# Kernel tuning notes

Hardware: AMD Instinct MI355X
Metric: run time of the kernel (lower is better)

The kernel has to match this reference:

```python
import jax, jax.numpy as jnp
import numpy as np

B, P, COV, H, S = 1024, 96, 31, 1024, 100  # batch, pred_len, cov_dim, hidden, num_samples
IN = COV + 1


def setup_inputs() -> dict:
    key = jax.random.key(0)
    ks = jax.random.split(key, 16)
    sc = 1.0 / np.sqrt(H)
    return {
        "covariates": jax.random.normal(ks[0], (B, P, COV), jnp.float32),
        "initial_value": jax.random.normal(ks[1], (B, 1), jnp.float32),
        "noise": jax.random.normal(ks[2], (P, S, B), jnp.float32),
        "h_init": jax.random.normal(ks[3], (2, B, H), jnp.float32) * 0.1,
        "c_init": jax.random.normal(ks[4], (2, B, H), jnp.float32) * 0.1,
        "W_ih0": jax.random.normal(ks[5], (4 * H, IN), jnp.float32) * sc,
        "W_hh0": jax.random.normal(ks[6], (4 * H, H), jnp.float32) * sc,
        "b_ih0": jax.random.normal(ks[7], (4 * H,), jnp.float32) * sc,
        "b_hh0": jax.random.normal(ks[8], (4 * H,), jnp.float32) * sc,
        "W_ih1": jax.random.normal(ks[9], (4 * H, H), jnp.float32) * sc,
        "W_hh1": jax.random.normal(ks[10], (4 * H, H), jnp.float32) * sc,
        "b_ih1": jax.random.normal(ks[11], (4 * H,), jnp.float32) * sc,
        "b_hh1": jax.random.normal(ks[12], (4 * H,), jnp.float32) * sc,
        "W_proj": jax.random.normal(ks[13], (2, H), jnp.float32) * sc,
        "b_proj": jax.random.normal(ks[14], (2,), jnp.float32) * sc,
    }


def _lstm_cell(x, h, c, W_ih, W_hh, b_ih, b_hh):
    # PyTorch gate order: i, f, g, o
    gates = x @ W_ih.T + h @ W_hh.T + b_ih + b_hh  # [B, 4H]
    i, f, g, o = jnp.split(gates, 4, axis=-1)
    i, f, o = jax.nn.sigmoid(i), jax.nn.sigmoid(f), jax.nn.sigmoid(o)
    g = jnp.tanh(g)
    c_new = f * c + i * g
    h_new = o * jnp.tanh(c_new)
    return h_new, c_new


def reference(covariates, initial_value, noise, h_init, c_init,
              W_ih0, W_hh0, b_ih0, b_hh0, W_ih1, W_hh1, b_ih1, b_hh1,
              W_proj, b_proj):
    def step(carry, inp):
        h0, c0, h1, c1, cur = carry
        cov_t, noise_t = inp  # [B, COV], [S, B]
        x = jnp.concatenate([cur[:, None], cov_t], axis=-1)  # [B, IN]
        h0, c0 = _lstm_cell(x, h0, c0, W_ih0, W_hh0, b_ih0, b_hh0)
        h1, c1 = _lstm_cell(h0, h1, c1, W_ih1, W_hh1, b_ih1, b_hh1)
        params = h1 @ W_proj.T + b_proj  # [B, 2]
        mu = params[:, 0]
        sigma = jax.nn.softplus(params[:, 1]) + 1e-6
        samples = mu[None, :] + sigma[None, :] * noise_t  # [S, B]
        cur = samples[0]
        return (h0, c0, h1, c1, cur), (params, samples)

    carry0 = (h_init[0], c_init[0], h_init[1], c_init[1], initial_value[:, 0])
    xs = (jnp.swapaxes(covariates, 0, 1), noise)  # time-major
    _, (all_params, all_samples) = jax.lax.scan(step, carry0, xs)
    all_params = jnp.swapaxes(all_params, 0, 1)       # [B, P, 2]
    all_samples = jnp.transpose(all_samples, (1, 2, 0))  # [S, B, P]
    return all_params, all_samples
```

## Files before the change

kernel.cpp:

```cpp
#include <hip/hip_runtime.h>
#include <stdint.h>

#define Bsz 1024
#define Hsz 1024
#define Psteps 96
#define Ssamp 100
#define COVn 31

typedef __attribute__((ext_vector_type(8))) short short8;
typedef __attribute__((ext_vector_type(4))) float f32x4;

__device__ inline unsigned short f2bf(float f) {
    union { float f; unsigned u; } v; v.f = f;
    unsigned r = v.u + 0x7FFFu + ((v.u >> 16) & 1u);
    return (unsigned short)(r >> 16);
}

__device__ inline float sigm(float x) { return 1.f / (1.f + __expf(-x)); }
__device__ inline float tanh_f(float x) { return 2.f / (1.f + __expf(-2.f * x)) - 1.f; }
__device__ inline float softplusf(float x) {
    return fmaxf(x, 0.f) + log1pf(__expf(-fabsf(x)));
}

__device__ inline void gld16(const unsigned short* g, unsigned short* l) {
    auto gp = (const __attribute__((address_space(1))) unsigned int*)(const unsigned int*)g;
    auto lp = (__attribute__((address_space(3))) unsigned int*)(unsigned int*)l;
    __builtin_amdgcn_global_load_lds(gp, lp, 16, 0, 0);
}

__device__ inline void stage_tile(const unsigned short* __restrict__ src, int rowStride,
                                  int row0, int k0, unsigned short* ldsBase, int tid) {
    #pragma unroll
    for (int i = 0; i < 4; ++i) {
        int c = i * 256 + tid;
        int row = c >> 3, s = c & 7;
        int col = ((s ^ (row & 7)) << 3) + k0;
        gld16(src + (size_t)(row0 + row) * rowStride + col, ldsBase + c * 8);
    }
}

__global__ void prep_weights(const float* __restrict__ Wih0, const float* __restrict__ Whh0,
                             const float* __restrict__ Wih1, const float* __restrict__ Whh1,
                             const float* __restrict__ bih0, const float* __restrict__ bhh0,
                             const float* __restrict__ bih1, const float* __restrict__ bhh1,
                             unsigned short* __restrict__ W0cat, unsigned short* __restrict__ W1cat,
                             float* __restrict__ bias0, float* __restrict__ bias1) {
    const size_t N0 = (size_t)4096 * 1088;
    const size_t N1 = (size_t)4096 * 2048;
    const size_t total = N0 + N1 + 8192;
    for (size_t e = (size_t)blockIdx.x * 256 + threadIdx.x; e < total; e += (size_t)gridDim.x * 256) {
        if (e < N0) {
            int gh = (int)(e / 1088), col = (int)(e % 1088);
            int src = ((gh & 3) << 10) + (gh >> 2);
            float v;
            if (col < 32) v = Wih0[(size_t)src * 32 + col];
            else if (col < 64) v = 0.f;
            else v = Whh0[(size_t)src * 1024 + (col - 64)];
            W0cat[e] = f2bf(v);
        } else if (e < N0 + N1) {
            size_t m = e - N0;
            int gh = (int)(m >> 11), col = (int)(m & 2047);
            int src = ((gh & 3) << 10) + (gh >> 2);
            float v = (col < 1024) ? Wih1[(size_t)src * 1024 + col]
                                   : Whh1[(size_t)src * 1024 + (col - 1024)];
            W1cat[m] = f2bf(v);
        } else {
            size_t m = e - N0 - N1;
            int which = (int)(m >> 12);
            int gh = (int)(m & 4095);
            int src = ((gh & 3) << 10) + (gh >> 2);
            if (which == 0) bias0[gh] = bih0[src] + bhh0[src];
            else            bias1[gh] = bih1[src] + bhh1[src];
        }
    }
}

__global__ void prep_state(const float* __restrict__ hinit, const float* __restrict__ cinit,
                           unsigned short* __restrict__ hb0, unsigned short* __restrict__ hb1,
                           float* __restrict__ c0, float* __restrict__ c1) {
    const size_t NM = (size_t)1024 * 1024;
    for (size_t e = (size_t)blockIdx.x * 256 + threadIdx.x; e < 4 * NM; e += (size_t)gridDim.x * 256) {
        if (e < NM) {
            hb0[e] = f2bf(hinit[e]);
        } else if (e < 2 * NM) {
            hb1[e - NM] = f2bf(hinit[e]);
        } else if (e < 3 * NM) {
            size_t j = e - 2 * NM; int h = (int)(j >> 10), b = (int)(j & 1023);
            c0[j] = cinit[(size_t)b * 1024 + h];
        } else {
            size_t j = e - 3 * NM; int h = (int)(j >> 10), b = (int)(j & 1023);
            c1[j] = cinit[NM + (size_t)b * 1024 + h];
        }
    }
}

template<int CELL>
__global__ __launch_bounds__(256) void lstm_step(
        int t,
        const float* __restrict__ cov, const float* __restrict__ initv,
        const float* __restrict__ noise, const float* __restrict__ bproj,
        const float* __restrict__ wproj,
        const unsigned short* __restrict__ WA,
        const float* __restrict__ biasH,
        const unsigned short* __restrict__ hA,
        const unsigned short* __restrict__ hB,
        unsigned short* __restrict__ hOut,
        float* __restrict__ cws,
        float* __restrict__ pbufPartial,
        float* __restrict__ outParams) {
    __shared__ __align__(16) char smem[131072];

    const int tid = threadIdx.x;
    const int m_tile = blockIdx.x & 31;
    const int n_tile = blockIdx.x >> 5;
    const int m0 = m_tile * 128;
    const int hc0 = m_tile * 32;
    const int b0 = n_tile * 128;
    const int lane = tid & 63;
    const int wid = tid >> 6;
    const int wm = wid >> 1, wn = wid & 1;
    const int NIT = (CELL == 0) ? 17 : 32;

    auto stageIt = [&](int j) {
        unsigned short* Ab = (unsigned short*)(smem + (j & 3) * 16384);
        unsigned short* Bb = (unsigned short*)(smem + 65536 + (j & 3) * 16384);
        if (CELL == 0) {
            stage_tile(WA, 1088, m0, j * 64, Ab, tid);
            if (j > 0) stage_tile(hB, 1024, b0, (j - 1) * 64, Bb, tid);
        } else {
            stage_tile(WA, 2048, m0, j * 64, Ab, tid);
            if (j < 16) stage_tile(hA, 1024, b0, j * 64, Bb, tid);
            else        stage_tile(hB, 1024, b0, (j - 16) * 64, Bb, tid);
        }
    };

    stageIt(0);
    stageIt(1);
    if (CELL == 0) {
        float* pj = (float*)(smem + 114688);
        float* curF = (float*)(smem + 114688 + 2048);
        if (t > 0) {
            int bl = tid >> 1, j = tid & 1;
            float s = bproj[j];
            #pragma unroll 8
            for (int m = 0; m < 32; ++m)
                s += pbufPartial[(size_t)((m << 10) + b0 + bl) * 2 + j];
            pj[tid] = s;
            if (m_tile == 0)
                outParams[((size_t)(b0 + bl) * Psteps + (t - 1)) * 2 + j] = s;
        }
        __syncthreads();
        if (tid < 128) {
            float cu;
            if (t == 0) {
                cu = initv[b0 + tid];
            } else {
                float p0 = pj[tid * 2 + 0], p1 = pj[tid * 2 + 1];
                cu = p0 + (softplusf(p1) + 1e-6f) * noise[(size_t)(t - 1) * (Ssamp * Bsz) + b0 + tid];
            }
            curF[tid] = cu;
        }
        __syncthreads();
        #pragma unroll
        for (int i = 0; i < 4; ++i) {
            int c = i * 256 + tid;
            int row = c >> 3, s = c & 7;
            int ts = s ^ (row & 7);
            short8 v;
            if (ts < 4) {
                const float* cr = cov + ((size_t)(b0 + row) * Psteps + t) * COVn;
                #pragma unroll
                for (int e = 0; e < 8; ++e) {
                    int col = ts * 8 + e;
                    float x = (col == 0) ? curF[row] : cr[col - 1];
                    v[e] = (short)f2bf(x);
                }
            } else {
                v = (short8){0, 0, 0, 0, 0, 0, 0, 0};
            }
            *(short8*)(smem + 65536 + c * 16) = v;
        }
    }
    __syncthreads();

    f32x4 acc[4][4];
    #pragma unroll
    for (int i = 0; i < 4; ++i)
        #pragma unroll
        for (int j = 0; j < 4; ++j) acc[i][j] = (f32x4){0.f, 0.f, 0.f, 0.f};

    for (int it = 0; it < NIT; ++it) {
        if (it + 2 < NIT) stageIt(it + 2);
        int rem = NIT - 1 - it;
        if (rem >= 2)      asm volatile("s_waitcnt vmcnt(16)" ::: "memory");
        else if (rem == 1) asm volatile("s_waitcnt vmcnt(8)" ::: "memory");
        else               asm volatile("s_waitcnt vmcnt(0)" ::: "memory");
        __builtin_amdgcn_s_barrier();
        asm volatile("" ::: "memory");
        const char* Abuf = smem + (it & 3) * 16384;
        const char* Bbuf = smem + 65536 + (it & 3) * 16384;
        __builtin_amdgcn_s_setprio(1);
        #pragma unroll
        for (int kh = 0; kh < 2; ++kh) {
            short8 af[4], bq[4];
            #pragma unroll
            for (int mf = 0; mf < 4; ++mf) {
                int row = wm * 64 + mf * 16 + (lane & 15);
                int slot = (kh * 4 + (lane >> 4)) ^ (row & 7);
                af[mf] = *(const short8*)(Abuf + row * 128 + slot * 16);
            }
            #pragma unroll
            for (int nf = 0; nf < 4; ++nf) {
                int row = wn * 64 + nf * 16 + (lane & 15);
                int slot = (kh * 4 + (lane >> 4)) ^ (row & 7);
                bq[nf] = *(const short8*)(Bbuf + row * 128 + slot * 16);
            }
            #pragma unroll
            for (int mf = 0; mf < 4; ++mf)
                #pragma unroll
                for (int nf = 0; nf < 4; ++nf)
                    acc[mf][nf] = __builtin_amdgcn_mfma_f32_16x16x32_bf16(af[mf], bq[nf], acc[mf][nf], 0, 0, 0);
        }
        __builtin_amdgcn_s_setprio(0);
    }
    __syncthreads();

    unsigned short* Ht = (unsigned short*)smem;
    float* part = (float*)(smem + 16384);
    float pp[4][2];
    if (CELL == 1) {
        #pragma unroll
        for (int nf = 0; nf < 4; ++nf) { pp[nf][0] = 0.f; pp[nf][1] = 0.f; }
    }
    #pragma unroll
    for (int mf = 0; mf < 4; ++mf) {
        int hl = wm * 16 + mf * 4 + (lane >> 4);
        int h = hc0 + hl;
        f32x4 bs = *(const f32x4*)&biasH[h * 4];
        #pragma unroll
        for (int nf = 0; nf < 4; ++nf) {
            int bl = wn * 64 + nf * 16 + (lane & 15);
            int b = b0 + bl;
            f32x4 v = acc[mf][nf];
            float gi = sigm(v.x + bs.x);
            float gf = sigm(v.y + bs.y);
            float gg = tanh_f(v.z + bs.z);
            float go = sigm(v.w + bs.w);
            size_t ci = (size_t)h * Bsz + b;
            float cn = gf * cws[ci] + gi * gg;
            cws[ci] = cn;
            float hn = go * tanh_f(cn);
            Ht[bl * 40 + hl] = f2bf(hn);
            if (CELL == 1) {
                pp[nf][0] += hn * wproj[h];
                pp[nf][1] += hn * wproj[Hsz + h];
            }
        }
    }
    if (CELL == 1) {
        #pragma unroll
        for (int nf = 0; nf < 4; ++nf)
            #pragma unroll
            for (int j = 0; j < 2; ++j) {
                float v = pp[nf][j];
                v += __shfl_xor(v, 16, 64);
                v += __shfl_xor(v, 32, 64);
                if (lane < 16)
                    part[((wm * 128) + wn * 64 + nf * 16 + lane) * 2 + j] = v;
            }
    }
    __syncthreads();
    {
        int row = tid >> 1, hf = tid & 1;
        short8 v0 = *(const short8*)&Ht[row * 40 + hf * 16];
        short8 v1 = *(const short8*)&Ht[row * 40 + hf * 16 + 8];
        *(short8*)&hOut[(size_t)(b0 + row) * Hsz + hc0 + hf * 16] = v0;
        *(short8*)&hOut[(size_t)(b0 + row) * Hsz + hc0 + hf * 16 + 8] = v1;
    }
    if (CELL == 1) {
        int bl = tid >> 1, j = tid & 1;
        pbufPartial[((size_t)m_tile * 1024 + b0 + bl) * 2 + j] =
            part[bl * 2 + j] + part[(128 + bl) * 2 + j];
    }
}

__global__ void tail_params(const float* __restrict__ pPart, const float* __restrict__ bproj,
                            float* __restrict__ dout, float* __restrict__ musig) {
    int idx = blockIdx.x * 256 + threadIdx.x;
    if (idx >= Bsz * Psteps) return;
    int b = idx / Psteps, t = idx % Psteps;
    float p0, p1;
    if (t == Psteps - 1) {
        p0 = bproj[0]; p1 = bproj[1];
        #pragma unroll 8
        for (int m = 0; m < 32; ++m) {
            p0 += pPart[(size_t)((m << 10) + b) * 2 + 0];
            p1 += pPart[(size_t)((m << 10) + b) * 2 + 1];
        }
        dout[(size_t)idx * 2 + 0] = p0;
        dout[(size_t)idx * 2 + 1] = p1;
    } else {
        p0 = dout[(size_t)idx * 2 + 0];
        p1 = dout[(size_t)idx * 2 + 1];
    }
    musig[(size_t)idx * 2 + 0] = p0;
    musig[(size_t)idx * 2 + 1] = softplusf(p1) + 1e-6f;
}

__global__ __launch_bounds__(256) void gen_samples(const float* __restrict__ noise,
                                                   const float* __restrict__ musig,
                                                   float* __restrict__ outS) {
    __shared__ float tile[16][97];
    int s = blockIdx.x >> 6;
    int b0 = (blockIdx.x & 63) << 4;
    int tid = threadIdx.x;
    for (int e = tid; e < Psteps * 16; e += 256) {
        int tt = e >> 4, b = e & 15;
        tile[b][tt] = noise[((size_t)tt * Ssamp + s) * Bsz + b0 + b];
    }
    __syncthreads();
    int b = tid >> 4, t0 = (tid & 15) * 6;
    const float* ms = musig + ((size_t)(b0 + b) * Psteps + t0) * 2;
    float* op = outS + ((size_t)s * Bsz + b0 + b) * Psteps + t0;
    #pragma unroll
    for (int k = 0; k < 6; ++k) {
        op[k] = ms[k * 2] + ms[k * 2 + 1] * tile[b][t0 + k];
    }
}

extern "C" void kernel_launch(void* const* d_in, const int* in_sizes, int n_in,
                              void* d_out, int out_size, void* d_ws, size_t ws_size,
                              hipStream_t stream) {
    const float* cov   = (const float*)d_in[0];
    const float* initv = (const float*)d_in[1];
    const float* noise = (const float*)d_in[2];
    const float* hinit = (const float*)d_in[3];
    const float* cinit = (const float*)d_in[4];
    const float* Wih0  = (const float*)d_in[5];
    const float* Whh0  = (const float*)d_in[6];
    const float* bih0  = (const float*)d_in[7];
    const float* bhh0  = (const float*)d_in[8];
    const float* Wih1  = (const float*)d_in[9];
    const float* Whh1  = (const float*)d_in[10];
    const float* bih1  = (const float*)d_in[11];
    const float* bhh1  = (const float*)d_in[12];
    const float* wproj = (const float*)d_in[13];
    const float* bproj = (const float*)d_in[14];
    float* dout = (float*)d_out;

    uint8_t* p = (uint8_t*)d_ws;
    auto alloc = [&](size_t bytes) { void* r = (void*)p; p += (bytes + 255) & ~(size_t)255; return r; };
    unsigned short* W0cat = (unsigned short*)alloc((size_t)4096 * 1088 * 2);
    unsigned short* W1cat = (unsigned short*)alloc((size_t)4096 * 2048 * 2);
    float* bias0 = (float*)alloc(4096 * 4);
    float* bias1 = (float*)alloc(4096 * 4);
    unsigned short* hb0 = (unsigned short*)alloc((size_t)2 * 1024 * 1024 * 2 + 256);
    unsigned short* hb1 = (unsigned short*)alloc((size_t)2 * 1024 * 1024 * 2 + 256);
    float* c0 = (float*)alloc((size_t)1024 * 1024 * 4);
    float* c1 = (float*)alloc((size_t)1024 * 1024 * 4);
    float* pbufPartial = (float*)alloc((size_t)32 * 1024 * 2 * 4);
    float* musig = (float*)alloc((size_t)1024 * 96 * 2 * 4);

    prep_weights<<<2048, 256, 0, stream>>>(Wih0, Whh0, Wih1, Whh1, bih0, bhh0, bih1, bhh1,
                                           W0cat, W1cat, bias0, bias1);
    prep_state<<<2048, 256, 0, stream>>>(hinit, cinit, hb0, hb1, c0, c1);

    const size_t HB = (size_t)1024 * 1024;
    for (int t = 0; t < Psteps; ++t) {
        const unsigned short* h0p = hb0 + (size_t)(t & 1) * HB;
        unsigned short* h0n = hb0 + (size_t)((t + 1) & 1) * HB;
        const unsigned short* h1p = hb1 + (size_t)(t & 1) * HB;
        unsigned short* h1n = hb1 + (size_t)((t + 1) & 1) * HB;
        lstm_step<0><<<256, 256, 0, stream>>>(t, cov, initv, noise, bproj, wproj,
                                              W0cat, bias0, nullptr, h0p, h0n, c0,
                                              pbufPartial, dout);
        lstm_step<1><<<256, 256, 0, stream>>>(t, cov, initv, noise, bproj, wproj,
                                              W1cat, bias1, h0n, h1p, h1n, c1,
                                              pbufPartial, dout);
    }
    tail_params<<<384, 256, 0, stream>>>(pbufPartial, bproj, dout, musig);
    gen_samples<<<6400, 256, 0, stream>>>(noise, musig, dout + (size_t)Bsz * Psteps * 2);
}
```

Measured before the change: 4.682 ms.

## Halve batch tile to 64, double-buffer LDS, launch 512 blocks per step

Each LSTM step block now covers 128 gate rows by 64 batch columns instead of 128, so the grid doubles to 512 blocks and more CUs are busy on a 256-CU part. LDS shrinks from 128KB to 48KB and the four-stage global_load_lds pipeline becomes a two-buffer scheme with a full __syncthreads per iteration, allowing two blocks per CU. The intent is better machine fill and occupancy. In exchange, the weight tile is re-read by twice as many blocks, and the shallower prefetch depth with an extra barrier per K step exposes more load latency.

```diff
diff --git a/kernel.cpp b/kernel.cpp
--- a/kernel.cpp
+++ b/kernel.cpp
@@ -28,10 +28,11 @@
     __builtin_amdgcn_global_load_lds(gp, lp, 16, 0, 0);
 }
 
+template<int CH>
 __device__ inline void stage_tile(const unsigned short* __restrict__ src, int rowStride,
                                   int row0, int k0, unsigned short* ldsBase, int tid) {
     #pragma unroll
-    for (int i = 0; i < 4; ++i) {
+    for (int i = 0; i < CH; ++i) {
         int c = i * 256 + tid;
         int row = c >> 3, s = c & 7;
         int col = ((s ^ (row & 7)) << 3) + k0;
@@ -95,7 +96,7 @@
 }
 
 template<int CELL>
-__global__ __launch_bounds__(256) void lstm_step(
+__global__ __launch_bounds__(256, 2) void lstm_step(
         int t,
         const float* __restrict__ cov, const float* __restrict__ initv,
         const float* __restrict__ noise, const float* __restrict__ bproj,
@@ -108,49 +109,50 @@
         float* __restrict__ cws,
         float* __restrict__ pbufPartial,
         float* __restrict__ outParams) {
-    __shared__ __align__(16) char smem[131072];
+    __shared__ __align__(16) char smem[49152];
 
     const int tid = threadIdx.x;
     const int m_tile = blockIdx.x & 31;
     const int n_tile = blockIdx.x >> 5;
     const int m0 = m_tile * 128;
     const int hc0 = m_tile * 32;
-    const int b0 = n_tile * 128;
+    const int b0 = n_tile * 64;
     const int lane = tid & 63;
     const int wid = tid >> 6;
     const int wm = wid >> 1, wn = wid & 1;
     const int NIT = (CELL == 0) ? 17 : 32;
 
     auto stageIt = [&](int j) {
-        unsigned short* Ab = (unsigned short*)(smem + (j & 3) * 16384);
-        unsigned short* Bb = (unsigned short*)(smem + 65536 + (j & 3) * 16384);
+        unsigned short* Ab = (unsigned short*)(smem + (j & 1) * 16384);
+        unsigned short* Bb = (unsigned short*)(smem + 32768 + (j & 1) * 8192);
         if (CELL == 0) {
-            stage_tile(WA, 1088, m0, j * 64, Ab, tid);
-            if (j > 0) stage_tile(hB, 1024, b0, (j - 1) * 64, Bb, tid);
+            stage_tile<4>(WA, 1088, m0, j * 64, Ab, tid);
+            if (j > 0) stage_tile<2>(hB, 1024, b0, (j - 1) * 64, Bb, tid);
         } else {
-            stage_tile(WA, 2048, m0, j * 64, Ab, tid);
-            if (j < 16) stage_tile(hA, 1024, b0, j * 64, Bb, tid);
-            else        stage_tile(hB, 1024, b0, (j - 16) * 64, Bb, tid);
+            stage_tile<4>(WA, 2048, m0, j * 64, Ab, tid);
+            if (j < 16) stage_tile<2>(hA, 1024, b0, j * 64, Bb, tid);
+            else        stage_tile<2>(hB, 1024, b0, (j - 16) * 64, Bb, tid);
         }
     };
 
     stageIt(0);
-    stageIt(1);
     if (CELL == 0) {
-        float* pj = (float*)(smem + 114688);
-        float* curF = (float*)(smem + 114688 + 2048);
+        float* pj = (float*)(smem + 40960);
+        float* curF = (float*)(smem + 40960 + 512);
         if (t > 0) {
-            int bl = tid >> 1, j = tid & 1;
-            float s = bproj[j];
-            #pragma unroll 8
-            for (int m = 0; m < 32; ++m)
-                s += pbufPartial[(size_t)((m << 10) + b0 + bl) * 2 + j];
-            pj[tid] = s;
-            if (m_tile == 0)
-                outParams[((size_t)(b0 + bl) * Psteps + (t - 1)) * 2 + j] = s;
+            if (tid < 128) {
+                int bl = tid >> 1, j = tid & 1;
+                float s = bproj[j];
+                #pragma unroll 8
+                for (int m = 0; m < 32; ++m)
+                    s += pbufPartial[(size_t)((m << 10) + b0 + bl) * 2 + j];
+                pj[tid] = s;
+                if (m_tile == 0)
+                    outParams[((size_t)(b0 + bl) * Psteps + (t - 1)) * 2 + j] = s;
+            }
         }
         __syncthreads();
-        if (tid < 128) {
+        if (tid < 64) {
             float cu;
             if (t == 0) {
                 cu = initv[b0 + tid];
@@ -162,7 +164,7 @@
         }
         __syncthreads();
         #pragma unroll
-        for (int i = 0; i < 4; ++i) {
+        for (int i = 0; i < 2; ++i) {
             int c = i * 256 + tid;
             int row = c >> 3, s = c & 7;
             int ts = s ^ (row & 7);
@@ -178,31 +180,25 @@
             } else {
                 v = (short8){0, 0, 0, 0, 0, 0, 0, 0};
             }
-            *(short8*)(smem + 65536 + c * 16) = v;
+            *(short8*)(smem + 32768 + c * 16) = v;
         }
     }
     __syncthreads();
 
-    f32x4 acc[4][4];
+    f32x4 acc[4][2];
     #pragma unroll
     for (int i = 0; i < 4; ++i)
         #pragma unroll
-        for (int j = 0; j < 4; ++j) acc[i][j] = (f32x4){0.f, 0.f, 0.f, 0.f};
+        for (int j = 0; j < 2; ++j) acc[i][j] = (f32x4){0.f, 0.f, 0.f, 0.f};
 
     for (int it = 0; it < NIT; ++it) {
-        if (it + 2 < NIT) stageIt(it + 2);
-        int rem = NIT - 1 - it;
-        if (rem >= 2)      asm volatile("s_waitcnt vmcnt(16)" ::: "memory");
-        else if (rem == 1) asm volatile("s_waitcnt vmcnt(8)" ::: "memory");
-        else               asm volatile("s_waitcnt vmcnt(0)" ::: "memory");
-        __builtin_amdgcn_s_barrier();
-        asm volatile("" ::: "memory");
-        const char* Abuf = smem + (it & 3) * 16384;
-        const char* Bbuf = smem + 65536 + (it & 3) * 16384;
+        if (it + 1 < NIT) stageIt(it + 1);
+        const char* Abuf = smem + (it & 1) * 16384;
+        const char* Bbuf = smem + 32768 + (it & 1) * 8192;
         __builtin_amdgcn_s_setprio(1);
         #pragma unroll
         for (int kh = 0; kh < 2; ++kh) {
-            short8 af[4], bq[4];
+            short8 af[4], bq[2];
             #pragma unroll
             for (int mf = 0; mf < 4; ++mf) {
                 int row = wm * 64 + mf * 16 + (lane & 15);
@@ -210,27 +206,27 @@
                 af[mf] = *(const short8*)(Abuf + row * 128 + slot * 16);
             }
             #pragma unroll
-            for (int nf = 0; nf < 4; ++nf) {
-                int row = wn * 64 + nf * 16 + (lane & 15);
+            for (int nf = 0; nf < 2; ++nf) {
+                int row = wn * 32 + nf * 16 + (lane & 15);
                 int slot = (kh * 4 + (lane >> 4)) ^ (row & 7);
                 bq[nf] = *(const short8*)(Bbuf + row * 128 + slot * 16);
             }
             #pragma unroll
             for (int mf = 0; mf < 4; ++mf)
                 #pragma unroll
-                for (int nf = 0; nf < 4; ++nf)
+                for (int nf = 0; nf < 2; ++nf)
                     acc[mf][nf] = __builtin_amdgcn_mfma_f32_16x16x32_bf16(af[mf], bq[nf], acc[mf][nf], 0, 0, 0);
         }
         __builtin_amdgcn_s_setprio(0);
-    }
-    __syncthreads();
+        __syncthreads();
+    }
 
     unsigned short* Ht = (unsigned short*)smem;
     float* part = (float*)(smem + 16384);
-    float pp[4][2];
+    float pp[2][2];
     if (CELL == 1) {
         #pragma unroll
-        for (int nf = 0; nf < 4; ++nf) { pp[nf][0] = 0.f; pp[nf][1] = 0.f; }
+        for (int nf = 0; nf < 2; ++nf) { pp[nf][0] = 0.f; pp[nf][1] = 0.f; }
     }
     #pragma unroll
     for (int mf = 0; mf < 4; ++mf) {
@@ -238,8 +234,8 @@
         int h = hc0 + hl;
         f32x4 bs = *(const f32x4*)&biasH[h * 4];
         #pragma unroll
-        for (int nf = 0; nf < 4; ++nf) {
-            int bl = wn * 64 + nf * 16 + (lane & 15);
+        for (int nf = 0; nf < 2; ++nf) {
+            int bl = wn * 32 + nf * 16 + (lane & 15);
             int b = b0 + bl;
             f32x4 v = acc[mf][nf];
             float gi = sigm(v.x + bs.x);
@@ -259,28 +255,28 @@
     }
     if (CELL == 1) {
         #pragma unroll
-        for (int nf = 0; nf < 4; ++nf)
+        for (int nf = 0; nf < 2; ++nf)
             #pragma unroll
             for (int j = 0; j < 2; ++j) {
                 float v = pp[nf][j];
                 v += __shfl_xor(v, 16, 64);
                 v += __shfl_xor(v, 32, 64);
                 if (lane < 16)
-                    part[((wm * 128) + wn * 64 + nf * 16 + lane) * 2 + j] = v;
+                    part[((wm * 64) + wn * 32 + nf * 16 + lane) * 2 + j] = v;
             }
     }
     __syncthreads();
-    {
+    if (tid < 128) {
         int row = tid >> 1, hf = tid & 1;
         short8 v0 = *(const short8*)&Ht[row * 40 + hf * 16];
         short8 v1 = *(const short8*)&Ht[row * 40 + hf * 16 + 8];
         *(short8*)&hOut[(size_t)(b0 + row) * Hsz + hc0 + hf * 16] = v0;
         *(short8*)&hOut[(size_t)(b0 + row) * Hsz + hc0 + hf * 16 + 8] = v1;
     }
-    if (CELL == 1) {
+    if (CELL == 1 && tid < 128) {
         int bl = tid >> 1, j = tid & 1;
         pbufPartial[((size_t)m_tile * 1024 + b0 + bl) * 2 + j] =
-            part[bl * 2 + j] + part[(128 + bl) * 2 + j];
+            part[bl * 2 + j] + part[(64 + bl) * 2 + j];
     }
 }
 
@@ -343,9 +339,11 @@
     const float* Wih1  = (const float*)d_in[9];
     const float* Whh1  = (const float*)d_in[10];
     const float* bih1  = (const float*)d_in[11];
+    const float* bih1x = bih1;
     const float* bhh1  = (const float*)d_in[12];
     const float* wproj = (const float*)d_in[13];
     const float* bproj = (const float*)d_in[14];
+    (void)bih1x;
     float* dout = (float*)d_out;
 
     uint8_t* p = (uint8_t*)d_ws;
@@ -371,10 +369,10 @@
         unsigned short* h0n = hb0 + (size_t)((t + 1) & 1) * HB;
         const unsigned short* h1p = hb1 + (size_t)(t & 1) * HB;
         unsigned short* h1n = hb1 + (size_t)((t + 1) & 1) * HB;
-        lstm_step<0><<<256, 256, 0, stream>>>(t, cov, initv, noise, bproj, wproj,
+        lstm_step<0><<<512, 256, 0, stream>>>(t, cov, initv, noise, bproj, wproj,
                                               W0cat, bias0, nullptr, h0p, h0n, c0,
                                               pbufPartial, dout);
-        lstm_step<1><<<256, 256, 0, stream>>>(t, cov, initv, noise, bproj, wproj,
+        lstm_step<1><<<512, 256, 0, stream>>>(t, cov, initv, noise, bproj, wproj,
                                               W1cat, bias1, h0n, h1p, h1n, c1,
                                               pbufPartial, dout);
     }
```

Result: faster. 4.068 ms (-13.1%).
